# Optimization experiments

Measured on AMD Instinct MI355X. Metric: run time of the kernel, lower is better.

## Reference

```python
import jax, jax.numpy as jnp
import numpy as np

ROUTINGS = 3
NUM_CAPSULES = 16


def squash(s, eps=1e-8):
    # s: [..., dim_capsule]
    norm = jnp.linalg.norm(s, axis=-1, keepdims=True)
    return (norm ** 2) / (1.0 + norm ** 2) * (s / (norm + eps))


def setup_inputs() -> dict:
    key = jax.random.key(0)
    k1, k2 = jax.random.split(key)
    x = jax.random.normal(k1, (64, 1024, 64), dtype=jnp.float32)      # [B, n_in, input_dim]
    weight = jax.random.normal(k2, (16, 64, 32), dtype=jnp.float32)    # [nc, input_dim, dc]
    return {"x": x, "weight": weight}


def reference(x, weight):
    B, n_in, _ = x.shape
    nc = weight.shape[0]
    # prediction vectors u_hat: [B, nc, n_in, dc]
    u_hat = jnp.einsum('bni,cid->bcnd', x, weight)
    # routing logits, softmax taken over the output-capsule axis (dim=1 in torch)
    b = jnp.zeros((B, nc, n_in, 1), dtype=u_hat.dtype)
    v = None
    for i in range(ROUTINGS):
        c = jax.nn.softmax(b, axis=1)                 # [B, nc, n_in, 1]
        s = jnp.sum(c * u_hat, axis=2)                # [B, nc, dc]
        v = squash(s)                                 # [B, nc, dc]
        if i < ROUTINGS - 1:
            # agreement: <u_hat, v> per input capsule
            b = b + jnp.einsum('bcnd,bcd->bcn', u_hat, v)[..., None]
    return v
```

## Files before the change

### kernel.cpp

```cpp
#include <hip/hip_runtime.h>
#include <math.h>

#define B_SZ 64
#define N_IN 1024
#define IDIM 64
#define NC   16
#define DC   32
#define NQ   4
#define QR   256
#define NTHR 1024
#define XS   260

typedef float f2 __attribute__((ext_vector_type(2)));

#define WS_CNT 0
#define WS_CS  1024
#define WS_SP1 17408
#define WS_SP2 279552

__device__ __forceinline__ void st_agent(float* p, float v) {
    __hip_atomic_store(p, v, __ATOMIC_RELAXED, __HIP_MEMORY_SCOPE_AGENT);
}
__device__ __forceinline__ float ld_agent(const float* p) {
    return __hip_atomic_load(p, __ATOMIC_RELAXED, __HIP_MEMORY_SCOPE_AGENT);
}
__device__ __forceinline__ float rdlane_f(float v, int l) {
    return __int_as_float(__builtin_amdgcn_readlane(__float_as_int(v), l));
}

__global__ __launch_bounds__(1024) void k_reset(int* cnt) {
    __hip_atomic_store(&cnt[threadIdx.x], 0, __ATOMIC_RELAXED, __HIP_MEMORY_SCOPE_AGENT);
}

__global__ __launch_bounds__(NTHR, 1)
void k_fused(const float* __restrict__ x, const float* __restrict__ W,
             float* __restrict__ out, int* __restrict__ cnt,
             float* __restrict__ cs, float* __restrict__ sp1, float* __restrict__ sp2) {
    const int b = blockIdx.x & 63, q = blockIdx.x >> 6;
    const int tid = threadIdx.x, lane = tid & 63, wave = tid >> 6;

    __shared__ float xT[IDIM * XS];
    __shared__ float aSm[NC * XS];
    __shared__ float pSm[4096];
    __shared__ float __align__(16) wSm[IDIM * 16];
    __shared__ float redSm[NC * IDIM];
    __shared__ float __align__(16) vSm[NC * 36];

    int* mycnt = &cnt[b * 16];
    auto arrive = [&]() {
        __syncthreads();
        if (tid == 0)
            __hip_atomic_fetch_add(mycnt, 1, __ATOMIC_RELEASE, __HIP_MEMORY_SCOPE_AGENT);
    };
    auto wait_ge = [&](int t) {
        if (tid == 0)
            while (__hip_atomic_load(mycnt, __ATOMIC_ACQUIRE,
                                     __HIP_MEMORY_SCOPE_AGENT) < t)
                __builtin_amdgcn_s_sleep(1);
        __syncthreads();
    };

    const float4* xb4 = reinterpret_cast<const float4*>(x + ((size_t)b * N_IN + q * QR) * IDIM);
#pragma unroll
    for (int m = 0; m < 4; m++) {
        const int f = tid + m * NTHR;
        const float4 v4 = xb4[f];
        const int n = f >> 4, i0 = (f & 15) * 4;
        xT[(i0 + 0) * XS + n] = v4.x;
        xT[(i0 + 1) * XS + n] = v4.y;
        xT[(i0 + 2) * XS + n] = v4.z;
        xT[(i0 + 3) * XS + n] = v4.w;
    }
    __syncthreads();

    {
        float s = 0.f;
#pragma unroll
        for (int j = 0; j < 4; j++) {
            const float4 v4 = *reinterpret_cast<const float4*>(&xT[lane * XS + wave * 16 + j * 4]);
            s += v4.x + v4.y + v4.z + v4.w;
        }
        redSm[wave * 64 + lane] = s;
    }
    __syncthreads();
    if (tid < 64) {
        float r = 0.f;
#pragma unroll
        for (int w2 = 0; w2 < 16; w2++) r += redSm[w2 * 64 + tid];
        st_agent(&cs[(b * NQ + q) * 64 + tid], r);
    }
    arrive();
    wait_ge(4);
    if (tid < 64) {
        float r = 0.f;
#pragma unroll
        for (int k = 0; k < NQ; k++) r += ld_agent(&cs[(b * NQ + k) * 64 + tid]);
        redSm[tid] = r;
    }
    __syncthreads();

    auto caps = [&](int mode) {
        if (tid < 512) {
            const int c = tid >> 5, dd = tid & 31;
            const float* Wc = W + c * (IDIM * DC) + dd;
            float s = 0.f;
#pragma unroll 8
            for (int i = 0; i < IDIM; i++) {
                const float rv = (mode == 0) ? redSm[i] : redSm[c * 64 + i];
                s += rv * Wc[i * DC];
            }
            if (mode == 0) s *= 0.0625f;
            float n2 = s * s;
#pragma unroll
            for (int m = 16; m >= 1; m >>= 1) n2 += __shfl_xor(n2, m);
            const float g = (n2 / (1.f + n2)) / (sqrtf(n2) + 1e-8f);
            if (mode == 2) { if (q == 0) out[b * (NC * DC) + c * DC + dd] = g * s; }
            else           vSm[c * 36 + dd] = g * s;
        }
        __syncthreads();
        if (mode == 2) return;
        const int i = tid >> 4, c = tid & 15;
        const float4* Wr = reinterpret_cast<const float4*>(W + (size_t)(c * IDIM + i) * DC);
        const float4* vv = reinterpret_cast<const float4*>(&vSm[c * 36]);
        float acc = 0.f;
#pragma unroll
        for (int dq = 0; dq < 8; dq++) {
            const float4 wq = Wr[dq], vq = vv[dq];
            acc += wq.x * vq.x + wq.y * vq.y + wq.z * vq.z + wq.w * vq.w;
        }
        if (mode == 0) wSm[i * 16 + c] = acc;
        else           wSm[i * 16 + c] += acc;
        __syncthreads();
    };

    auto route = [&](float* sp) {
        const int row = tid & 255, grp = tid >> 8;
        {
            f2 a01 = {0.f, 0.f}, a23 = {0.f, 0.f};
#pragma unroll 8
            for (int i = 0; i < IDIM; i++) {
                const float xv = xT[i * XS + row];
                const float4 w4 = *reinterpret_cast<const float4*>(&wSm[i * 16 + grp * 4]);
                const f2 xv2 = {xv, xv};
                a01 += xv2 * (f2){w4.x, w4.y};
                a23 += xv2 * (f2){w4.z, w4.w};
            }
            aSm[(grp * 4 + 0) * XS + row] = a01.x;
            aSm[(grp * 4 + 1) * XS + row] = a01.y;
            aSm[(grp * 4 + 2) * XS + row] = a23.x;
            aSm[(grp * 4 + 3) * XS + row] = a23.y;
        }
        __syncthreads();
        float cw0, cw1, cw2, cw3;
        {
            float av[NC];
#pragma unroll
            for (int k = 0; k < NC; k++) av[k] = aSm[((k + grp * 4) & 15) * XS + row];
            float mx = av[0];
#pragma unroll
            for (int k = 1; k < NC; k++) mx = fmaxf(mx, av[k]);
            float ss = 0.f;
#pragma unroll
            for (int k = 0; k < NC; k++) { av[k] = __expf(av[k] - mx); ss += av[k]; }
            const float inv = 1.f / ss;
            cw0 = av[0] * inv; cw1 = av[1] * inv; cw2 = av[2] * inv; cw3 = av[3] * inv;
        }
        {
            const int cg = wave >> 2, rq = wave & 3;
            float a0 = 0.f, a1 = 0.f, a2 = 0.f, a3 = 0.f;
#pragma unroll
            for (int j = 0; j < 16; j++) {
                const float4 xv = *reinterpret_cast<const float4*>(
                    &xT[lane * XS + rq * 64 + j * 4]);
#pragma unroll
                for (int l = 0; l < 4; l++) {
                    const int nl = j * 4 + l;
                    const float xc = (l == 0) ? xv.x : (l == 1) ? xv.y
                                   : (l == 2) ? xv.z : xv.w;
                    a0 += rdlane_f(cw0, nl) * xc;
                    a1 += rdlane_f(cw1, nl) * xc;
                    a2 += rdlane_f(cw2, nl) * xc;
                    a3 += rdlane_f(cw3, nl) * xc;
                }
            }
            pSm[rq * 1024 + (cg * 4 + 0) * 64 + lane] = a0;
            pSm[rq * 1024 + (cg * 4 + 1) * 64 + lane] = a1;
            pSm[rq * 1024 + (cg * 4 + 2) * 64 + lane] = a2;
            pSm[rq * 1024 + (cg * 4 + 3) * 64 + lane] = a3;
        }
        __syncthreads();
        const float val = pSm[tid] + pSm[1024 + tid] + pSm[2048 + tid] + pSm[3072 + tid];
        st_agent(&sp[(size_t)(b * NQ + q) * 1024 + tid], val);
    };

    caps(0);
    route(sp1);
    arrive();
    wait_ge(8);
    {
        float r = 0.f;
#pragma unroll
        for (int k = 0; k < NQ; k++) r += ld_agent(&sp1[(size_t)(b * NQ + k) * 1024 + tid]);
        redSm[tid] = r;
    }
    __syncthreads();
    caps(1);
    route(sp2);
    arrive();
    if (q != 0) return;
    wait_ge(12);
    {
        float r = 0.f;
#pragma unroll
        for (int k = 0; k < NQ; k++) r += ld_agent(&sp2[(size_t)(b * NQ + k) * 1024 + tid]);
        redSm[tid] = r;
    }
    __syncthreads();
    caps(2);
}

extern "C" void kernel_launch(void* const* d_in, const int* in_sizes, int n_in,
                              void* d_out, int out_size, void* d_ws, size_t ws_size,
                              hipStream_t stream) {
    const float* x = (const float*)d_in[0];
    const float* W = (const float*)d_in[1];
    float* out = (float*)d_out;
    float* ws = (float*)d_ws;

    int*   cnt = (int*)(ws + WS_CNT);
    float* cs  = ws + WS_CS;
    float* sp1 = ws + WS_SP1;
    float* sp2 = ws + WS_SP2;

    k_reset<<<1, 1024, 0, stream>>>(cnt);
    k_fused<<<B_SZ * NQ, NTHR, 0, stream>>>(x, W, out, cnt, cs, sp1, sp2);
}
```

Measured before the change: 52.01 us.

## Store x tile row-major and broadcast routing weights via readlane

New measurement: 49.92 us. 4.0% less time.

```diff
diff --git a/kernel.cpp b/kernel.cpp
--- a/kernel.cpp
+++ b/kernel.cpp
@@ -9,9 +9,8 @@
 #define NQ   4
 #define QR   256
 #define NTHR 1024
-#define XS   260
-
-typedef float f2 __attribute__((ext_vector_type(2)));
+#define XS   68
+#define AS   20
 
 #define WS_CNT 0
 #define WS_CS  1024
@@ -38,11 +37,13 @@
              float* __restrict__ cs, float* __restrict__ sp1, float* __restrict__ sp2) {
     const int b = blockIdx.x & 63, q = blockIdx.x >> 6;
     const int tid = threadIdx.x, lane = tid & 63, wave = tid >> 6;
-
-    __shared__ float xT[IDIM * XS];
-    __shared__ float aSm[NC * XS];
-    __shared__ float pSm[4096];
-    __shared__ float __align__(16) wSm[IDIM * 16];
+    const int row = tid & 255, grp = tid >> 8;
+    const int rq = wave & 3;
+
+    __shared__ float __align__(16) xT[QR * XS];
+    __shared__ float __align__(16) aSmT[QR * AS];
+    __shared__ float __align__(16) pSm[4 * 64 * AS];
+    __shared__ float __align__(16) wSm[IDIM * AS];
     __shared__ float redSm[NC * IDIM];
     __shared__ float __align__(16) vSm[NC * 36];
 
@@ -66,20 +67,14 @@
         const int f = tid + m * NTHR;
         const float4 v4 = xb4[f];
         const int n = f >> 4, i0 = (f & 15) * 4;
-        xT[(i0 + 0) * XS + n] = v4.x;
-        xT[(i0 + 1) * XS + n] = v4.y;
-        xT[(i0 + 2) * XS + n] = v4.z;
-        xT[(i0 + 3) * XS + n] = v4.w;
+        *reinterpret_cast<float4*>(&xT[n * XS + i0]) = v4;
     }
     __syncthreads();
 
     {
         float s = 0.f;
 #pragma unroll
-        for (int j = 0; j < 4; j++) {
-            const float4 v4 = *reinterpret_cast<const float4*>(&xT[lane * XS + wave * 16 + j * 4]);
-            s += v4.x + v4.y + v4.z + v4.w;
-        }
+        for (int t = 0; t < 16; t++) s += xT[(wave * 16 + t) * XS + lane];
         redSm[wave * 64 + lane] = s;
     }
     __syncthreads();
@@ -128,34 +123,41 @@
             const float4 wq = Wr[dq], vq = vv[dq];
             acc += wq.x * vq.x + wq.y * vq.y + wq.z * vq.z + wq.w * vq.w;
         }
-        if (mode == 0) wSm[i * 16 + c] = acc;
-        else           wSm[i * 16 + c] += acc;
-        __syncthreads();
-    };
-
-    auto route = [&](float* sp) {
-        const int row = tid & 255, grp = tid >> 8;
+        if (mode == 0) wSm[i * AS + c] = acc;
+        else           wSm[i * AS + c] += acc;
+        __syncthreads();
+    };
+
+    auto route = [&](float* sp) -> float {
+        const float4 wr4 = *reinterpret_cast<const float4*>(&wSm[lane * AS + grp * 4]);
         {
-            f2 a01 = {0.f, 0.f}, a23 = {0.f, 0.f};
-#pragma unroll 8
-            for (int i = 0; i < IDIM; i++) {
-                const float xv = xT[i * XS + row];
-                const float4 w4 = *reinterpret_cast<const float4*>(&wSm[i * 16 + grp * 4]);
-                const f2 xv2 = {xv, xv};
-                a01 += xv2 * (f2){w4.x, w4.y};
-                a23 += xv2 * (f2){w4.z, w4.w};
+            float a0 = 0.f, a1 = 0.f, a2 = 0.f, a3 = 0.f;
+#pragma unroll
+            for (int iq = 0; iq < 16; iq++) {
+                const float4 xv = *reinterpret_cast<const float4*>(&xT[row * XS + iq * 4]);
+#pragma unroll
+                for (int j = 0; j < 4; j++) {
+                    const int i = iq * 4 + j;
+                    const float xc = (j == 0) ? xv.x : (j == 1) ? xv.y
+                                   : (j == 2) ? xv.z : xv.w;
+                    a0 += rdlane_f(wr4.x, i) * xc;
+                    a1 += rdlane_f(wr4.y, i) * xc;
+                    a2 += rdlane_f(wr4.z, i) * xc;
+                    a3 += rdlane_f(wr4.w, i) * xc;
+                }
             }
-            aSm[(grp * 4 + 0) * XS + row] = a01.x;
-            aSm[(grp * 4 + 1) * XS + row] = a01.y;
-            aSm[(grp * 4 + 2) * XS + row] = a23.x;
-            aSm[(grp * 4 + 3) * XS + row] = a23.y;
+            *reinterpret_cast<float4*>(&aSmT[row * AS + grp * 4]) =
+                make_float4(a0, a1, a2, a3);
         }
         __syncthreads();
         float cw0, cw1, cw2, cw3;
         {
-            float av[NC];
-#pragma unroll
-            for (int k = 0; k < NC; k++) av[k] = aSm[((k + grp * 4) & 15) * XS + row];
+            const float4 q0 = *reinterpret_cast<const float4*>(&aSmT[row * AS + 0]);
+            const float4 q1 = *reinterpret_cast<const float4*>(&aSmT[row * AS + 4]);
+            const float4 q2 = *reinterpret_cast<const float4*>(&aSmT[row * AS + 8]);
+            const float4 q3 = *reinterpret_cast<const float4*>(&aSmT[row * AS + 12]);
+            float av[NC] = {q0.x, q0.y, q0.z, q0.w, q1.x, q1.y, q1.z, q1.w,
+                            q2.x, q2.y, q2.z, q2.w, q3.x, q3.y, q3.z, q3.w};
             float mx = av[0];
 #pragma unroll
             for (int k = 1; k < NC; k++) mx = fmaxf(mx, av[k]);
@@ -163,56 +165,56 @@
 #pragma unroll
             for (int k = 0; k < NC; k++) { av[k] = __expf(av[k] - mx); ss += av[k]; }
             const float inv = 1.f / ss;
-            cw0 = av[0] * inv; cw1 = av[1] * inv; cw2 = av[2] * inv; cw3 = av[3] * inv;
+            if (grp == 0)      { cw0 = av[0];  cw1 = av[1];  cw2 = av[2];  cw3 = av[3];  }
+            else if (grp == 1) { cw0 = av[4];  cw1 = av[5];  cw2 = av[6];  cw3 = av[7];  }
+            else if (grp == 2) { cw0 = av[8];  cw1 = av[9];  cw2 = av[10]; cw3 = av[11]; }
+            else               { cw0 = av[12]; cw1 = av[13]; cw2 = av[14]; cw3 = av[15]; }
+            cw0 *= inv; cw1 *= inv; cw2 *= inv; cw3 *= inv;
         }
         {
-            const int cg = wave >> 2, rq = wave & 3;
-            float a0 = 0.f, a1 = 0.f, a2 = 0.f, a3 = 0.f;
-#pragma unroll
-            for (int j = 0; j < 16; j++) {
-                const float4 xv = *reinterpret_cast<const float4*>(
-                    &xT[lane * XS + rq * 64 + j * 4]);
-#pragma unroll
-                for (int l = 0; l < 4; l++) {
-                    const int nl = j * 4 + l;
-                    const float xc = (l == 0) ? xv.x : (l == 1) ? xv.y
-                                   : (l == 2) ? xv.z : xv.w;
-                    a0 += rdlane_f(cw0, nl) * xc;
-                    a1 += rdlane_f(cw1, nl) * xc;
-                    a2 += rdlane_f(cw2, nl) * xc;
-                    a3 += rdlane_f(cw3, nl) * xc;
-                }
+            float s0 = 0.f, s1 = 0.f, s2 = 0.f, s3 = 0.f;
+#pragma unroll
+            for (int nl = 0; nl < 64; nl++) {
+                const float xv = xT[(rq * 64 + nl) * XS + lane];
+                s0 += rdlane_f(cw0, nl) * xv;
+                s1 += rdlane_f(cw1, nl) * xv;
+                s2 += rdlane_f(cw2, nl) * xv;
+                s3 += rdlane_f(cw3, nl) * xv;
             }
-            pSm[rq * 1024 + (cg * 4 + 0) * 64 + lane] = a0;
-            pSm[rq * 1024 + (cg * 4 + 1) * 64 + lane] = a1;
-            pSm[rq * 1024 + (cg * 4 + 2) * 64 + lane] = a2;
-            pSm[rq * 1024 + (cg * 4 + 3) * 64 + lane] = a3;
-        }
-        __syncthreads();
-        const float val = pSm[tid] + pSm[1024 + tid] + pSm[2048 + tid] + pSm[3072 + tid];
+            *reinterpret_cast<float4*>(&pSm[(rq * 64 + lane) * AS + grp * 4]) =
+                make_float4(s0, s1, s2, s3);
+        }
+        __syncthreads();
+        const float val = pSm[(0 * 64 + lane) * AS + wave] +
+                          pSm[(1 * 64 + lane) * AS + wave] +
+                          pSm[(2 * 64 + lane) * AS + wave] +
+                          pSm[(3 * 64 + lane) * AS + wave];
         st_agent(&sp[(size_t)(b * NQ + q) * 1024 + tid], val);
+        return val;
     };
 
     caps(0);
-    route(sp1);
+    const float v1 = route(sp1);
     arrive();
     wait_ge(8);
     {
-        float r = 0.f;
-#pragma unroll
-        for (int k = 0; k < NQ; k++) r += ld_agent(&sp1[(size_t)(b * NQ + k) * 1024 + tid]);
+        float r = v1;
+#pragma unroll
+        for (int k = 0; k < NQ; k++)
+            if (k != q) r += ld_agent(&sp1[(size_t)(b * NQ + k) * 1024 + tid]);
         redSm[tid] = r;
     }
     __syncthreads();
     caps(1);
-    route(sp2);
+    const float v2 = route(sp2);
     arrive();
     if (q != 0) return;
     wait_ge(12);
     {
-        float r = 0.f;
-#pragma unroll
-        for (int k = 0; k < NQ; k++) r += ld_agent(&sp2[(size_t)(b * NQ + k) * 1024 + tid]);
+        float r = v2;
+#pragma unroll
+        for (int k = 0; k < NQ; k++)
+            if (k != q) r += ld_agent(&sp2[(size_t)(b * NQ + k) * 1024 + tid]);
         redSm[tid] = r;
     }
     __syncthreads();
```
